# Performance work log

Measured on AMD Instinct MI355X. Metric: run time of the kernel, lower is better.

Reference implementation:

```python
import jax, jax.numpy as jnp
import numpy as np

N = 50000      # nodes
E = 800000     # edges (avg degree 16)
D_IN = 64
D_H = 128
D_OUT = 10
EPS = 1e-8


def setup_inputs() -> dict:
    key = jax.random.key(0)
    ks = jax.random.split(key, 6)
    x = jax.random.normal(ks[0], (N, D_IN), dtype=jnp.float32)
    edge_index = jax.random.randint(ks[1], (2, E), 0, N, dtype=jnp.int32)
    # weights act on homogeneous-augmented features (d_in + 1)
    W_self0 = jax.random.normal(ks[2], (D_IN + 1, D_H), jnp.float32) / np.sqrt(D_IN + 1)
    W_neigh0 = jax.random.normal(ks[3], (D_IN + 1, D_H), jnp.float32) / np.sqrt(D_IN + 1)
    W_self1 = jax.random.normal(ks[4], (D_H + 1, D_OUT), jnp.float32) / np.sqrt(D_H + 1)
    W_neigh1 = jax.random.normal(ks[5], (D_H + 1, D_OUT), jnp.float32) / np.sqrt(D_H + 1)
    return {"x": x, "edge_index": edge_index,
            "W_self0": W_self0, "W_neigh0": W_neigh0,
            "W_self1": W_self1, "W_neigh1": W_neigh1}


def _projective_sage_layer(h, src, dst, W_self, W_neigh, last):
    n = h.shape[0]
    # lift to projective (homogeneous) coordinates: append ones column
    hh = jnp.concatenate([h, jnp.ones((n, 1), h.dtype)], axis=1)  # [N, d+1]
    # mean-aggregate neighbor messages (irregular gather + segment-sum)
    msg_sum = jax.ops.segment_sum(hh[src], dst, num_segments=n)   # [N, d+1]
    deg = jax.ops.segment_sum(jnp.ones((src.shape[0],), h.dtype), dst, num_segments=n)
    neigh = msg_sum / jnp.maximum(deg, 1.0)[:, None]
    out = hh @ W_self + neigh @ W_neigh                           # [N, d_out]
    # projective normalization (points on unit sphere of projective space)
    out = out / (jnp.linalg.norm(out, axis=1, keepdims=True) + EPS)
    return out if last else jax.nn.relu(out)


def reference(x, edge_index, W_self0, W_neigh0, W_self1, W_neigh1):
    src, dst = edge_index[0], edge_index[1]
    h = _projective_sage_layer(x, src, dst, W_self0, W_neigh0, last=False)
    h = _projective_sage_layer(h, src, dst, W_self1, W_neigh1, last=True)
    return jax.nn.log_softmax(h, axis=1)
```

## Files before the change

### kernel.cpp

```cpp
#include <hip/hip_runtime.h>
#include <hip/hip_bf16.h>
#include <math.h>

#define EPSN 1e-8f
#define MAXBUCK 512

typedef __attribute__((ext_vector_type(8))) short short8;
typedef __attribute__((ext_vector_type(4))) float f32x4;

static __device__ __forceinline__ unsigned short f2bf(float f) {
    union { float f; unsigned int u; } v; v.f = f;
    unsigned int u = v.u;
    return (unsigned short)((u + 0x7fffu + ((u >> 16) & 1u)) >> 16);
}
static __device__ __forceinline__ float bf2f(unsigned short h) {
    union { unsigned int u; float f; } v; v.u = ((unsigned int)h) << 16;
    return v.f;
}
static __device__ __forceinline__ unsigned int pk2(float a, float b) {
    return (((unsigned int)f2bf(b)) << 16) | (unsigned int)f2bf(a);
}

__global__ void fused_pre(const int* __restrict__ dst, int* __restrict__ ghist, int E, int nbuck,
                          const float* __restrict__ Ws0, const float* __restrict__ Wn0,
                          const float* __restrict__ Ws1, const float* __restrict__ Wn1,
                          unsigned short* __restrict__ B0t, unsigned short* __restrict__ B1t,
                          float* __restrict__ bias,
                          const float* __restrict__ x, unsigned short* __restrict__ A0, int N,
                          int histB, int prepB) {
    int b = blockIdx.x;
    if (b < histB) {
        __shared__ int h[MAXBUCK];
        for (int i = threadIdx.x; i < MAXBUCK; i += 256) h[i] = 0;
        __syncthreads();
        int CH = (E + histB - 1) / histB;
        int lo = b * CH, hi = min(E, lo + CH);
        for (int e = lo + (int)threadIdx.x; e < hi; e += 256) atomicAdd(&h[dst[e] >> 7], 1);
        __syncthreads();
        for (int i = threadIdx.x; i < nbuck; i += 256) if (h[i]) atomicAdd(&ghist[i], h[i]);
        return;
    }
    if (b < histB + prepB) {
        int t = (b - histB) * 256 + threadIdx.x;
        if (t < 128 * 160) {
            int n = t / 160, k = t % 160;
            float v = 0.f;
            if (k < 64) v = Ws0[k * 128 + n];
            else if (k < 128) v = Wn0[(k - 64) * 128 + n];
            else if (k == 128) v = Ws0[64 * 128 + n];
            else if (k == 129) v = Wn0[64 * 128 + n];
            B0t[n * 160 + k] = f2bf(v);
        }
        int u = t - 128 * 160;
        if (u >= 0 && u < 32 * 128) {
            int c = u / 128, k = u % 128;
            float v = 0.f;
            if (c < 10) v = Ws1[k * 10 + c];
            else if (c < 20) v = Wn1[k * 10 + (c - 10)];
            B1t[c * 128 + k] = f2bf(v);
        }
        int w = t - 128 * 160 - 32 * 128;
        if (w >= 0 && w < 20) bias[w] = (w < 10) ? Ws1[128 * 10 + w] : Wn1[128 * 10 + (w - 10)];
        return;
    }
    int u = (b - histB - prepB) * 256 + threadIdx.x;
    if (u >= N * 8) return;
    int n = u >> 3, s = u & 7;
    const float4* xp = (const float4*)(x + (size_t)n * 64 + s * 8);
    float4 v0 = xp[0], v1 = xp[1];
    short8 r;
    r[0] = (short)f2bf(v0.x); r[1] = (short)f2bf(v0.y);
    r[2] = (short)f2bf(v0.z); r[3] = (short)f2bf(v0.w);
    r[4] = (short)f2bf(v1.x); r[5] = (short)f2bf(v1.y);
    r[6] = (short)f2bf(v1.z); r[7] = (short)f2bf(v1.w);
    *(short8*)(&A0[(size_t)n * 160 + s * 8]) = r;
}

__global__ void bucket_scan(const int* __restrict__ ghist, int* __restrict__ boff,
                            int* __restrict__ bcur, int nbuck, int E,
                            int* __restrict__ row_ptr, int N) {
    __shared__ int bufa[MAXBUCK], bufb[MAXBUCK];
    int t = threadIdx.x;
    int v = (t < nbuck) ? ghist[t] : 0;
    bufa[t] = v;
    __syncthreads();
    int* cur = bufa; int* nxt = bufb;
    for (int off = 1; off < MAXBUCK; off <<= 1) {
        int xv = cur[t];
        if (t >= off) xv += cur[t - off];
        nxt[t] = xv;
        __syncthreads();
        int* tmp = cur; cur = nxt; nxt = tmp;
    }
    int incl = cur[t];
    int excl = incl - v;
    if (t < nbuck) { boff[t] = excl; bcur[t] = excl; }
    if (t == nbuck - 1) boff[nbuck] = incl;
    if (t == 0) row_ptr[N] = E;
}

__global__ void bucket_scatter(const int* __restrict__ src, const int* __restrict__ dst,
                               int* __restrict__ bcur, unsigned int* __restrict__ pairs,
                               int E) {
    __shared__ int h[MAXBUCK];
    __shared__ int bs[MAXBUCK];
    for (int i = threadIdx.x; i < MAXBUCK; i += 256) h[i] = 0;
    __syncthreads();
    int CH = (E + gridDim.x - 1) / gridDim.x;
    int lo = blockIdx.x * CH, hi = min(E, lo + CH);
    for (int e = lo + (int)threadIdx.x; e < hi; e += 256) atomicAdd(&h[dst[e] >> 7], 1);
    __syncthreads();
    for (int i = threadIdx.x; i < MAXBUCK; i += 256) {
        int c = h[i];
        bs[i] = c ? atomicAdd(&bcur[i], c) : 0;
        h[i] = 0;
    }
    __syncthreads();
    for (int e = lo + (int)threadIdx.x; e < hi; e += 256) {
        int d = dst[e];
        int b = d >> 7;
        int idx = atomicAdd(&h[b], 1);
        pairs[bs[b] + idx] = (((unsigned int)(d & 127)) << 16) | (unsigned int)src[e];
    }
}

__global__ void csr_finalize(const unsigned int* __restrict__ pairs, const int* __restrict__ boff,
                             int* __restrict__ row_ptr, unsigned short* __restrict__ col,
                             int N) {
    __shared__ int lh[128], ls[128], lc[128];
    int b = blockIdx.x, t = threadIdx.x;
    int lo = boff[b], hi = boff[b + 1];
    for (int i = t; i < 128; i += 256) lh[i] = 0;
    __syncthreads();
    for (int e = lo + t; e < hi; e += 256) atomicAdd(&lh[pairs[e] >> 16], 1);
    __syncthreads();
    if (t < 128) {
        int v = lh[t];
        int incl = v;
#pragma unroll
        for (int off = 1; off < 64; off <<= 1) {
            int y = __shfl_up(incl, off);
            if ((t & 63) >= off) incl += y;
        }
        ls[t] = incl;
    }
    __syncthreads();
    if (t < 128) {
        int v = lh[t];
        int excl = ls[t] - v + ((t >= 64) ? ls[63] : 0);
        int node = b * 128 + t;
        if (node < N) row_ptr[node] = lo + excl;
        lc[t] = excl;
    }
    __syncthreads();
    for (int e = lo + t; e < hi; e += 256) {
        unsigned int p = pairs[e];
        int ld = p >> 16;
        int idx = atomicAdd(&lc[ld], 1);
        col[lo + idx] = (unsigned short)(p & 0xFFFFu);
    }
}

__global__ void agg0_kernel(const int* __restrict__ row_ptr, const unsigned short* __restrict__ col,
                            unsigned short* __restrict__ A0, int N) {
    int n = (int)((blockIdx.x * blockDim.x + threadIdx.x) >> 6);
    if (n >= N) return;
    int lane = threadIdx.x & 63;
    int rs = row_ptr[n], re = row_ptr[n + 1];
    float acc = 0.f;
    for (int base = rs; base < re; base += 64) {
        int cnt = min(64, re - base);
        int e = 0;
        if (base + lane < re) e = (int)col[base + lane];
        int j = 0;
        for (; j + 16 <= cnt; j += 16) {
            float v[16];
#pragma unroll
            for (int i = 0; i < 16; ++i) {
                int s = __shfl(e, j + i);
                v[i] = bf2f(A0[(size_t)s * 160 + lane]);
            }
#pragma unroll
            for (int i = 0; i < 16; ++i) acc += v[i];
        }
        for (; j + 4 <= cnt; j += 4) {
            float v[4];
#pragma unroll
            for (int i = 0; i < 4; ++i) {
                int s = __shfl(e, j + i);
                v[i] = bf2f(A0[(size_t)s * 160 + lane]);
            }
#pragma unroll
            for (int i = 0; i < 4; ++i) acc += v[i];
        }
        for (; j < cnt; ++j) {
            int s = __shfl(e, j);
            acc += bf2f(A0[(size_t)s * 160 + lane]);
        }
    }
    float deg = (float)(re - rs);
    float scale = 1.0f / fmaxf(deg, 1.0f);
    unsigned short* row = A0 + (size_t)n * 160;
    row[64 + lane] = f2bf(acc * scale);
    if (lane == 0) *(unsigned int*)(&row[128]) = pk2(1.0f, deg * scale);
    if (lane >= 1 && lane < 16) *(unsigned int*)(&row[128 + lane * 2]) = 0u;
}

__global__ void __launch_bounds__(256)
gemm0_kernel(const unsigned short* __restrict__ A0, const unsigned short* __restrict__ B0t,
             unsigned short* __restrict__ h1, int N) {
    __shared__ unsigned short As[64 * 168];
    __shared__ unsigned short Bs[128 * 168];
    int t = threadIdx.x, blk = blockIdx.x;
    for (int i = t; i < 128 * 20; i += 256) {
        int r = i / 20, c = i % 20;
        *(uint4*)(&Bs[r * 168 + c * 8]) = *(const uint4*)(&B0t[r * 160 + c * 8]);
    }
    for (int i = t; i < 64 * 20; i += 256) {
        int r = i / 20, c = i % 20;
        int gr = blk * 64 + r;
        uint4 v = {0, 0, 0, 0};
        if (gr < N) v = *(const uint4*)(&A0[(size_t)gr * 160 + c * 8]);
        *(uint4*)(&As[r * 168 + c * 8]) = v;
    }
    __syncthreads();

    int wave = t >> 6, lane = t & 63;
    int lo = lane & 15, hi = lane >> 4;
    f32x4 acc[8];
#pragma unroll
    for (int f = 0; f < 8; ++f) acc[f] = (f32x4){0.f, 0.f, 0.f, 0.f};

#pragma unroll
    for (int ks = 0; ks < 5; ++ks) {
        short8 a = *(const short8*)(&As[(wave * 16 + lo) * 168 + ks * 32 + hi * 8]);
#pragma unroll
        for (int f = 0; f < 8; ++f) {
            short8 b = *(const short8*)(&Bs[(f * 16 + lo) * 168 + ks * 32 + hi * 8]);
            acc[f] = __builtin_amdgcn_mfma_f32_16x16x32_bf16(a, b, acc[f], 0, 0, 0);
        }
    }
#pragma unroll
    for (int j = 0; j < 4; ++j) {
        float s = 0.f;
#pragma unroll
        for (int f = 0; f < 8; ++f) s += acc[f][j] * acc[f][j];
#pragma unroll
        for (int m = 1; m < 16; m <<= 1) s += __shfl_xor(s, m);
        float inv = 1.0f / (sqrtf(s) + EPSN);
        int gr = blk * 64 + wave * 16 + hi * 4 + j;
        if (gr < N) {
#pragma unroll
            for (int f = 0; f < 8; ++f)
                h1[(size_t)gr * 128 + f * 16 + lo] = f2bf(fmaxf(acc[f][j] * inv, 0.f));
        }
    }
}

__global__ void __launch_bounds__(256)
gemm1_kernel(const unsigned short* __restrict__ h1, const unsigned short* __restrict__ B1t,
             const float* __restrict__ bias, float* __restrict__ S, float* __restrict__ Qp, int N) {
    __shared__ unsigned short As[128 * 136];
    __shared__ unsigned short Bs[32 * 136];
    int t = threadIdx.x, blk = blockIdx.x;
    for (int i = t; i < 32 * 16; i += 256) {
        int r = i / 16, c = i % 16;
        *(uint4*)(&Bs[r * 136 + c * 8]) = *(const uint4*)(&B1t[r * 128 + c * 8]);
    }
    for (int i = t; i < 128 * 16; i += 256) {
        int r = i / 16, c = i % 16;
        int gr = blk * 128 + r;
        uint4 v = {0, 0, 0, 0};
        if (gr < N) v = *(const uint4*)(&h1[(size_t)gr * 128 + c * 8]);
        *(uint4*)(&As[r * 136 + c * 8]) = v;
    }
    __syncthreads();

    int wave = t >> 6, lane = t & 63, lo = lane & 15, hi = lane >> 4;
    f32x4 acc[2][2];
#pragma unroll
    for (int m = 0; m < 2; ++m) { acc[m][0] = (f32x4){0,0,0,0}; acc[m][1] = (f32x4){0,0,0,0}; }

#pragma unroll
    for (int ks = 0; ks < 4; ++ks) {
        short8 b0 = *(const short8*)(&Bs[lo * 136 + ks * 32 + hi * 8]);
        short8 b1 = *(const short8*)(&Bs[(16 + lo) * 136 + ks * 32 + hi * 8]);
#pragma unroll
        for (int m = 0; m < 2; ++m) {
            short8 a = *(const short8*)(&As[(wave * 32 + m * 16 + lo) * 136 + ks * 32 + hi * 8]);
            acc[m][0] = __builtin_amdgcn_mfma_f32_16x16x32_bf16(a, b0, acc[m][0], 0, 0, 0);
            acc[m][1] = __builtin_amdgcn_mfma_f32_16x16x32_bf16(a, b1, acc[m][1], 0, 0, 0);
        }
    }
#pragma unroll
    for (int m = 0; m < 2; ++m)
#pragma unroll
        for (int j = 0; j < 4; ++j) {
            int gr = blk * 128 + wave * 32 + m * 16 + hi * 4 + j;
            if (gr < N) {
                float v0 = acc[m][0][j] + bias[lo];
                if (lo < 10) S[(size_t)gr * 10 + lo] = v0;
                else         Qp[(size_t)gr * 16 + (lo - 10)] = v0;
                if (lo < 4)       Qp[(size_t)gr * 16 + 6 + lo] = acc[m][1][j] + bias[16 + lo];
                else if (lo < 10) Qp[(size_t)gr * 16 + 6 + lo] = 0.f;
            }
        }
}

__global__ void final_kernel(const float* __restrict__ S, const float* __restrict__ Qp,
                             const int* __restrict__ row_ptr, const unsigned short* __restrict__ col,
                             float* __restrict__ out, int N) {
    int n = blockIdx.x * blockDim.x + threadIdx.x;
    if (n >= N) return;
    int rs = row_ptr[n], re = row_ptr[n + 1];
    float q0 = 0.f, q1 = 0.f, q2 = 0.f, q3 = 0.f, q4 = 0.f;
    float q5 = 0.f, q6 = 0.f, q7 = 0.f, q8 = 0.f, q9 = 0.f;
    int e = rs;
    for (; e + 3 < re; e += 4) {
        float4 a[4], b[4]; float2 t2[4];
#pragma unroll
        for (int i = 0; i < 4; ++i) {
            int c = (int)col[e + i];
            const float4* r = (const float4*)(&Qp[(size_t)c * 16]);
            a[i] = r[0]; b[i] = r[1];
            t2[i] = *(const float2*)(&Qp[(size_t)c * 16 + 8]);
        }
#pragma unroll
        for (int i = 0; i < 4; ++i) {
            q0 += a[i].x; q1 += a[i].y; q2 += a[i].z; q3 += a[i].w;
            q4 += b[i].x; q5 += b[i].y; q6 += b[i].z; q7 += b[i].w;
            q8 += t2[i].x; q9 += t2[i].y;
        }
    }
    for (; e < re; ++e) {
        int c0 = (int)col[e];
        const float4* r0 = (const float4*)(&Qp[(size_t)c0 * 16]);
        float4 a0 = r0[0], b0 = r0[1];
        float2 t0 = *(const float2*)(&Qp[(size_t)c0 * 16 + 8]);
        q0 += a0.x; q1 += a0.y; q2 += a0.z; q3 += a0.w;
        q4 += b0.x; q5 += b0.y; q6 += b0.z; q7 += b0.w;
        q8 += t0.x; q9 += t0.y;
    }
    float deg = (float)(re - rs);
    float scale = 1.0f / fmaxf(deg, 1.0f);
    const float* Sr = &S[(size_t)n * 10];
    float p[10];
    p[0] = Sr[0] + q0 * scale; p[1] = Sr[1] + q1 * scale;
    p[2] = Sr[2] + q2 * scale; p[3] = Sr[3] + q3 * scale;
    p[4] = Sr[4] + q4 * scale; p[5] = Sr[5] + q5 * scale;
    p[6] = Sr[6] + q6 * scale; p[7] = Sr[7] + q7 * scale;
    p[8] = Sr[8] + q8 * scale; p[9] = Sr[9] + q9 * scale;
    float ss = 0.f;
#pragma unroll
    for (int j = 0; j < 10; ++j) ss = fmaf(p[j], p[j], ss);
    float inv = 1.0f / (sqrtf(ss) + EPSN);
    float m = -INFINITY;
#pragma unroll
    for (int j = 0; j < 10; ++j) { p[j] *= inv; m = fmaxf(m, p[j]); }
    float se = 0.f;
#pragma unroll
    for (int j = 0; j < 10; ++j) se += expf(p[j] - m);
    float ls = logf(se) + m;
#pragma unroll
    for (int j = 0; j < 10; ++j) out[(size_t)n * 10 + j] = p[j] - ls;
}

extern "C" void kernel_launch(void* const* d_in, const int* in_sizes, int n_in,
                              void* d_out, int out_size, void* d_ws, size_t ws_size,
                              hipStream_t stream) {
    const float* x   = (const float*)d_in[0];
    const int*   ei  = (const int*)d_in[1];
    const float* Ws0 = (const float*)d_in[2];
    const float* Wn0 = (const float*)d_in[3];
    const float* Ws1 = (const float*)d_in[4];
    const float* Wn1 = (const float*)d_in[5];

    int N = in_sizes[0] / 64;
    int E = in_sizes[1] / 2;
    const int* src = ei;
    const int* dst = ei + E;
    int nbuck = (N + 127) / 128;

    char* ws = (char*)d_ws;
    size_t off = 0;
    unsigned short* A0   = (unsigned short*)(ws + off); off += (size_t)N * 160 * 2;
    unsigned short* h1   = (unsigned short*)(ws + off); off += (size_t)N * 128 * 2;
    float*          S    = (float*)(ws + off);          off += (size_t)N * 10 * 4;
    float*          Qp   = (float*)(ws + off);          off += (size_t)N * 16 * 4;
    unsigned short* B0t  = (unsigned short*)(ws + off); off += 128 * 160 * 2;
    unsigned short* B1t  = (unsigned short*)(ws + off); off += 32 * 128 * 2;
    float*          bias = (float*)(ws + off);          off += 128;
    int*            rowp = (int*)(ws + off);            off += ((size_t)N + 4) * 4;
    unsigned short* colb = (unsigned short*)(ws + off); off += ((size_t)E + 8) * 2;
    unsigned int*   pairs= (unsigned int*)(ws + off);   off += (size_t)E * 4;
    int*            ghist= (int*)(ws + off);            off += MAXBUCK * 4;
    int*            boff = (int*)(ws + off);            off += (MAXBUCK + 1) * 4;
    int*            bcur = (int*)(ws + off);            off += MAXBUCK * 4;
    float* outp = (float*)d_out;

    int histB = 256;
    int prepB = (128 * 160 + 32 * 128 + 20 + 255) / 256;
    int xcvB  = (N * 8 + 255) / 256;

    hipMemsetAsync(ghist, 0, MAXBUCK * 4, stream);
    fused_pre<<<histB + prepB + xcvB, 256, 0, stream>>>(
        dst, ghist, E, nbuck, Ws0, Wn0, Ws1, Wn1, B0t, B1t, bias, x, A0, N, histB, prepB);
    bucket_scan   <<<1, MAXBUCK, 0, stream>>>(ghist, boff, bcur, nbuck, E, rowp, N);
    bucket_scatter<<<256, 256, 0, stream>>>(src, dst, bcur, pairs, E);
    csr_finalize  <<<nbuck, 256, 0, stream>>>(pairs, boff, rowp, colb, N);

    agg0_kernel <<<(N + 3) / 4, 256, 0, stream>>>(rowp, colb, A0, N);
    gemm0_kernel<<<(N + 63) / 64, 256, 0, stream>>>(A0, B0t, h1, N);
    gemm1_kernel<<<(N + 127) / 128, 256, 0, stream>>>(h1, B1t, bias, S, Qp, N);
    final_kernel<<<(N + 255) / 256, 256, 0, stream>>>(S, Qp, rowp, colb, outp, N);
}
```

Measured before the change: 176.5 us.

## Fuse two GEMM layers via LDS and reuse per-block histograms in scatter

```diff
diff --git a/kernel.cpp b/kernel.cpp
--- a/kernel.cpp
+++ b/kernel.cpp
@@ -4,6 +4,7 @@
 
 #define EPSN 1e-8f
 #define MAXBUCK 512
+#define HISTB 512
 
 typedef __attribute__((ext_vector_type(8))) short short8;
 typedef __attribute__((ext_vector_type(4))) float f32x4;
@@ -21,27 +22,32 @@
     return (((unsigned int)f2bf(b)) << 16) | (unsigned int)f2bf(a);
 }
 
-__global__ void fused_pre(const int* __restrict__ dst, int* __restrict__ ghist, int E, int nbuck,
+__global__ void fused_pre(const int* __restrict__ dst, int* __restrict__ ghist,
+                          int* __restrict__ phist, int E, int nbuck,
                           const float* __restrict__ Ws0, const float* __restrict__ Wn0,
                           const float* __restrict__ Ws1, const float* __restrict__ Wn1,
                           unsigned short* __restrict__ B0t, unsigned short* __restrict__ B1t,
                           float* __restrict__ bias,
                           const float* __restrict__ x, unsigned short* __restrict__ A0, int N,
-                          int histB, int prepB) {
+                          int prepB) {
     int b = blockIdx.x;
-    if (b < histB) {
+    if (b < HISTB) {
         __shared__ int h[MAXBUCK];
         for (int i = threadIdx.x; i < MAXBUCK; i += 256) h[i] = 0;
         __syncthreads();
-        int CH = (E + histB - 1) / histB;
+        int CH = (E + HISTB - 1) / HISTB;
         int lo = b * CH, hi = min(E, lo + CH);
         for (int e = lo + (int)threadIdx.x; e < hi; e += 256) atomicAdd(&h[dst[e] >> 7], 1);
         __syncthreads();
-        for (int i = threadIdx.x; i < nbuck; i += 256) if (h[i]) atomicAdd(&ghist[i], h[i]);
+        for (int i = threadIdx.x; i < MAXBUCK; i += 256) {
+            int c = h[i];
+            phist[b * MAXBUCK + i] = c;
+            if (c && i < nbuck) atomicAdd(&ghist[i], c);
+        }
         return;
     }
-    if (b < histB + prepB) {
-        int t = (b - histB) * 256 + threadIdx.x;
+    if (b < HISTB + prepB) {
+        int t = (b - HISTB) * 256 + threadIdx.x;
         if (t < 128 * 160) {
             int n = t / 160, k = t % 160;
             float v = 0.f;
@@ -63,7 +69,7 @@
         if (w >= 0 && w < 20) bias[w] = (w < 10) ? Ws1[128 * 10 + w] : Wn1[128 * 10 + (w - 10)];
         return;
     }
-    int u = (b - histB - prepB) * 256 + threadIdx.x;
+    int u = (b - HISTB - prepB) * 256 + threadIdx.x;
     if (u >= N * 8) return;
     int n = u >> 3, s = u & 7;
     const float4* xp = (const float4*)(x + (size_t)n * 64 + s * 8);
@@ -100,27 +106,25 @@
 }
 
 __global__ void bucket_scatter(const int* __restrict__ src, const int* __restrict__ dst,
+                               const int* __restrict__ phist,
                                int* __restrict__ bcur, unsigned int* __restrict__ pairs,
                                int E) {
     __shared__ int h[MAXBUCK];
     __shared__ int bs[MAXBUCK];
-    for (int i = threadIdx.x; i < MAXBUCK; i += 256) h[i] = 0;
-    __syncthreads();
-    int CH = (E + gridDim.x - 1) / gridDim.x;
-    int lo = blockIdx.x * CH, hi = min(E, lo + CH);
-    for (int e = lo + (int)threadIdx.x; e < hi; e += 256) atomicAdd(&h[dst[e] >> 7], 1);
-    __syncthreads();
+    int b = blockIdx.x;
     for (int i = threadIdx.x; i < MAXBUCK; i += 256) {
-        int c = h[i];
+        int c = phist[b * MAXBUCK + i];
         bs[i] = c ? atomicAdd(&bcur[i], c) : 0;
         h[i] = 0;
     }
     __syncthreads();
+    int CH = (E + HISTB - 1) / HISTB;
+    int lo = b * CH, hi = min(E, lo + CH);
     for (int e = lo + (int)threadIdx.x; e < hi; e += 256) {
         int d = dst[e];
-        int b = d >> 7;
-        int idx = atomicAdd(&h[b], 1);
-        pairs[bs[b] + idx] = (((unsigned int)(d & 127)) << 16) | (unsigned int)src[e];
+        int bkt = d >> 7;
+        int idx = atomicAdd(&h[bkt], 1);
+        pairs[bs[bkt] + idx] = (((unsigned int)(d & 127)) << 16) | (unsigned int)src[e];
     }
 }
 
@@ -207,8 +211,9 @@
 }
 
 __global__ void __launch_bounds__(256)
-gemm0_kernel(const unsigned short* __restrict__ A0, const unsigned short* __restrict__ B0t,
-             unsigned short* __restrict__ h1, int N) {
+gemm01_kernel(const unsigned short* __restrict__ A0, const unsigned short* __restrict__ B0t,
+              const unsigned short* __restrict__ B1t, const float* __restrict__ bias,
+              float* __restrict__ S, float* __restrict__ Qp, int N) {
     __shared__ unsigned short As[64 * 168];
     __shared__ unsigned short Bs[128 * 168];
     int t = threadIdx.x, blk = blockIdx.x;
@@ -240,6 +245,9 @@
             acc[f] = __builtin_amdgcn_mfma_f32_16x16x32_bf16(a, b, acc[f], 0, 0, 0);
         }
     }
+    __syncthreads();
+
+    unsigned short* h1s = As;
 #pragma unroll
     for (int j = 0; j < 4; ++j) {
         float s = 0.f;
@@ -248,63 +256,38 @@
 #pragma unroll
         for (int m = 1; m < 16; m <<= 1) s += __shfl_xor(s, m);
         float inv = 1.0f / (sqrtf(s) + EPSN);
-        int gr = blk * 64 + wave * 16 + hi * 4 + j;
-        if (gr < N) {
-#pragma unroll
-            for (int f = 0; f < 8; ++f)
-                h1[(size_t)gr * 128 + f * 16 + lo] = f2bf(fmaxf(acc[f][j] * inv, 0.f));
-        }
-    }
-}
-
-__global__ void __launch_bounds__(256)
-gemm1_kernel(const unsigned short* __restrict__ h1, const unsigned short* __restrict__ B1t,
-             const float* __restrict__ bias, float* __restrict__ S, float* __restrict__ Qp, int N) {
-    __shared__ unsigned short As[128 * 136];
-    __shared__ unsigned short Bs[32 * 136];
-    int t = threadIdx.x, blk = blockIdx.x;
+        int r = wave * 16 + hi * 4 + j;
+#pragma unroll
+        for (int f = 0; f < 8; ++f)
+            h1s[r * 136 + f * 16 + lo] = f2bf(fmaxf(acc[f][j] * inv, 0.f));
+    }
     for (int i = t; i < 32 * 16; i += 256) {
         int r = i / 16, c = i % 16;
         *(uint4*)(&Bs[r * 136 + c * 8]) = *(const uint4*)(&B1t[r * 128 + c * 8]);
     }
-    for (int i = t; i < 128 * 16; i += 256) {
-        int r = i / 16, c = i % 16;
-        int gr = blk * 128 + r;
-        uint4 v = {0, 0, 0, 0};
-        if (gr < N) v = *(const uint4*)(&h1[(size_t)gr * 128 + c * 8]);
-        *(uint4*)(&As[r * 136 + c * 8]) = v;
-    }
-    __syncthreads();
-
-    int wave = t >> 6, lane = t & 63, lo = lane & 15, hi = lane >> 4;
-    f32x4 acc[2][2];
-#pragma unroll
-    for (int m = 0; m < 2; ++m) { acc[m][0] = (f32x4){0,0,0,0}; acc[m][1] = (f32x4){0,0,0,0}; }
-
+    __syncthreads();
+
+    f32x4 c0 = (f32x4){0.f, 0.f, 0.f, 0.f};
+    f32x4 c1 = (f32x4){0.f, 0.f, 0.f, 0.f};
 #pragma unroll
     for (int ks = 0; ks < 4; ++ks) {
         short8 b0 = *(const short8*)(&Bs[lo * 136 + ks * 32 + hi * 8]);
         short8 b1 = *(const short8*)(&Bs[(16 + lo) * 136 + ks * 32 + hi * 8]);
-#pragma unroll
-        for (int m = 0; m < 2; ++m) {
-            short8 a = *(const short8*)(&As[(wave * 32 + m * 16 + lo) * 136 + ks * 32 + hi * 8]);
-            acc[m][0] = __builtin_amdgcn_mfma_f32_16x16x32_bf16(a, b0, acc[m][0], 0, 0, 0);
-            acc[m][1] = __builtin_amdgcn_mfma_f32_16x16x32_bf16(a, b1, acc[m][1], 0, 0, 0);
-        }
-    }
-#pragma unroll
-    for (int m = 0; m < 2; ++m)
-#pragma unroll
-        for (int j = 0; j < 4; ++j) {
-            int gr = blk * 128 + wave * 32 + m * 16 + hi * 4 + j;
-            if (gr < N) {
-                float v0 = acc[m][0][j] + bias[lo];
-                if (lo < 10) S[(size_t)gr * 10 + lo] = v0;
-                else         Qp[(size_t)gr * 16 + (lo - 10)] = v0;
-                if (lo < 4)       Qp[(size_t)gr * 16 + 6 + lo] = acc[m][1][j] + bias[16 + lo];
-                else if (lo < 10) Qp[(size_t)gr * 16 + 6 + lo] = 0.f;
-            }
-        }
+        short8 a  = *(const short8*)(&h1s[(wave * 16 + lo) * 136 + ks * 32 + hi * 8]);
+        c0 = __builtin_amdgcn_mfma_f32_16x16x32_bf16(a, b0, c0, 0, 0, 0);
+        c1 = __builtin_amdgcn_mfma_f32_16x16x32_bf16(a, b1, c1, 0, 0, 0);
+    }
+#pragma unroll
+    for (int j = 0; j < 4; ++j) {
+        int gr = blk * 64 + wave * 16 + hi * 4 + j;
+        if (gr < N) {
+            float v0 = c0[j] + bias[lo];
+            if (lo < 10) S[(size_t)gr * 10 + lo] = v0;
+            else         Qp[(size_t)gr * 16 + (lo - 10)] = v0;
+            if (lo < 4)       Qp[(size_t)gr * 16 + 6 + lo] = c1[j] + bias[16 + lo];
+            else if (lo < 10) Qp[(size_t)gr * 16 + 6 + lo] = 0.f;
+        }
+    }
 }
 
 __global__ void final_kernel(const float* __restrict__ S, const float* __restrict__ Qp,
@@ -384,7 +367,6 @@
     char* ws = (char*)d_ws;
     size_t off = 0;
     unsigned short* A0   = (unsigned short*)(ws + off); off += (size_t)N * 160 * 2;
-    unsigned short* h1   = (unsigned short*)(ws + off); off += (size_t)N * 128 * 2;
     float*          S    = (float*)(ws + off);          off += (size_t)N * 10 * 4;
     float*          Qp   = (float*)(ws + off);          off += (size_t)N * 16 * 4;
     unsigned short* B0t  = (unsigned short*)(ws + off); off += 128 * 160 * 2;
@@ -394,23 +376,22 @@
     unsigned short* colb = (unsigned short*)(ws + off); off += ((size_t)E + 8) * 2;
     unsigned int*   pairs= (unsigned int*)(ws + off);   off += (size_t)E * 4;
     int*            ghist= (int*)(ws + off);            off += MAXBUCK * 4;
+    int*            phist= (int*)(ws + off);            off += (size_t)HISTB * MAXBUCK * 4;
     int*            boff = (int*)(ws + off);            off += (MAXBUCK + 1) * 4;
     int*            bcur = (int*)(ws + off);            off += MAXBUCK * 4;
     float* outp = (float*)d_out;
 
-    int histB = 256;
     int prepB = (128 * 160 + 32 * 128 + 20 + 255) / 256;
     int xcvB  = (N * 8 + 255) / 256;
 
     hipMemsetAsync(ghist, 0, MAXBUCK * 4, stream);
-    fused_pre<<<histB + prepB + xcvB, 256, 0, stream>>>(
-        dst, ghist, E, nbuck, Ws0, Wn0, Ws1, Wn1, B0t, B1t, bias, x, A0, N, histB, prepB);
+    fused_pre<<<HISTB + prepB + xcvB, 256, 0, stream>>>(
+        dst, ghist, phist, E, nbuck, Ws0, Wn0, Ws1, Wn1, B0t, B1t, bias, x, A0, N, prepB);
     bucket_scan   <<<1, MAXBUCK, 0, stream>>>(ghist, boff, bcur, nbuck, E, rowp, N);
-    bucket_scatter<<<256, 256, 0, stream>>>(src, dst, bcur, pairs, E);
+    bucket_scatter<<<HISTB, 256, 0, stream>>>(src, dst, phist, bcur, pairs, E);
     csr_finalize  <<<nbuck, 256, 0, stream>>>(pairs, boff, rowp, colb, N);
 
     agg0_kernel <<<(N + 3) / 4, 256, 0, stream>>>(rowp, colb, A0, N);
-    gemm0_kernel<<<(N + 63) / 64, 256, 0, stream>>>(A0, B0t, h1, N);
-    gemm1_kernel<<<(N + 127) / 128, 256, 0, stream>>>(h1, B1t, bias, S, Qp, N);
+    gemm01_kernel<<<(N + 63) / 64, 256, 0, stream>>>(A0, B0t, B1t, bias, S, Qp, N);
     final_kernel<<<(N + 255) / 256, 256, 0, stream>>>(S, Qp, rowp, colb, outp, N);
 }
```

After: 188.7 us. 1.07x slower.
